# Performance work log

Hardware: AMD Instinct MI355X
Metric: run time of the kernel (lower is better)

## Reference

```python
import jax, jax.numpy as jnp
import numpy as np

ROI = 7      # pooled output size
S = 5        # max adaptive samples per bin dim (boxes <= 0.25*120=30px -> ceil(30/7)=5)


def _roi_align(f, boxes):
    """torchvision roi_align, aligned=True, sampling_ratio=-1 (adaptive).
    f: [C,H,W]; boxes: [N,4] normalized xywh. Returns [N,C,ROI,ROI]."""
    C, H, W = f.shape
    fH, fW = jnp.float32(H), jnp.float32(W)
    x1 = boxes[:, 0] * fW - 0.5                 # aligned=True offset
    y1 = boxes[:, 1] * fH - 0.5
    roi_w = boxes[:, 2] * fW
    roi_h = boxes[:, 3] * fH
    bin_w = roi_w / ROI
    bin_h = roi_h / ROI
    gw = jnp.maximum(jnp.ceil(roi_w / ROI), 1.0)   # adaptive grid counts [N]
    gh = jnp.maximum(jnp.ceil(roi_h / ROI), 1.0)
    ph = jnp.arange(ROI, dtype=jnp.float32)
    s = jnp.arange(S, dtype=jnp.float32)
    # sample coords [N, ROI, S]
    ys = y1[:, None, None] + ph[None, :, None] * bin_h[:, None, None] \
         + (s[None, None, :] + 0.5) * bin_h[:, None, None] / gh[:, None, None]
    xs = x1[:, None, None] + ph[None, :, None] * bin_w[:, None, None] \
         + (s[None, None, :] + 0.5) * bin_w[:, None, None] / gw[:, None, None]
    # broadcast to [N, ROI, ROI, S, S]
    y = ys[:, :, None, :, None]
    x = xs[:, None, :, None, :]
    m = ((s[None, None, None, :, None] < gh[:, None, None, None, None]) &
         (s[None, None, None, None, :] < gw[:, None, None, None, None]))
    valid = (y > -1.0) & (y < fH) & (x > -1.0) & (x < fW)
    yc = jnp.clip(y, 0.0, fH - 1.0)
    xc = jnp.clip(x, 0.0, fW - 1.0)
    y0 = jnp.floor(yc).astype(jnp.int32)
    x0 = jnp.floor(xc).astype(jnp.int32)
    yh = jnp.minimum(y0 + 1, H - 1)
    xh = jnp.minimum(x0 + 1, W - 1)
    ly = yc - y0.astype(jnp.float32); hy = 1.0 - ly
    lx = xc - x0.astype(jnp.float32); hx = 1.0 - lx
    scale = (valid & m).astype(f.dtype)
    y = jnp.broadcast_to(y0 * 0, (boxes.shape[0], ROI, ROI, S, S))  # shape anchor (unused)
    w00 = (hy * hx * scale)[None]
    w01 = (hy * lx * scale)[None]
    w10 = (ly * hx * scale)[None]
    w11 = (ly * lx * scale)[None]
    # gathered values: [C, N, ROI, ROI, S, S]
    vals = (w00 * f[:, y0, x0] + w01 * f[:, y0, xh] +
            w10 * f[:, yh, x0] + w11 * f[:, yh, xh])
    count = (gh * gw)[None, :, None, None]
    pooled = vals.sum(axis=(-1, -2)) / count        # [C, N, ROI, ROI]
    return pooled.transpose(1, 0, 2, 3)              # [N, C, ROI, ROI]


def setup_inputs() -> dict:
    key = jax.random.key(0)
    k = jax.random.split(key, 6)
    features = jax.random.normal(k[0], (1, 128, 120, 120), jnp.float32)
    u = jax.random.uniform(k[1], (512, 4), jnp.float32)
    boxes = jnp.stack([u[:, 0] * 0.7, u[:, 1] * 0.7,
                       0.05 + 0.2 * u[:, 2], 0.05 + 0.2 * u[:, 3]], axis=1)
    d_in = 128 * ROI * ROI  # 6272
    W1 = jax.random.normal(k[2], (d_in, 512), jnp.float32) / np.float32(np.sqrt(d_in))
    b1 = jax.random.normal(k[3], (512,), jnp.float32) * 0.01
    W2 = jax.random.normal(k[4], (512, 256), jnp.float32) / np.float32(np.sqrt(512))
    b2 = jax.random.normal(k[5], (256,), jnp.float32) * 0.01
    return {"features": features, "boxes": boxes, "W1": W1, "b1": b1, "W2": W2, "b2": b2}


def reference(features, boxes, W1, b1, W2, b2):
    roi = _roi_align(features[0], boxes)             # [N,128,7,7]
    flat = roi.reshape(roi.shape[0], -1)             # [N,6272] channel-major like torch .view
    h = jax.nn.relu(flat @ W1 + b1)                  # dropout in eval mode = identity
    return h @ W2 + b2                               # [N,256]
```

## Files before the change

### kernel.cpp

```cpp
#include <hip/hip_runtime.h>
#include <hip/hip_bf16.h>
#include <stdint.h>

#define DI __device__ __forceinline__

typedef __attribute__((ext_vector_type(8))) short short8;
typedef __attribute__((ext_vector_type(4))) float f32x4;

constexpr int CH   = 128;
constexpr int FH   = 120;
constexpr int FW   = 120;
constexpr int NBOX = 512;
constexpr int KDIM = 49 * 128;
constexpr int D1   = 512;
constexpr int D2   = 256;
constexpr int SPLITS = 14;
constexpr int KC     = KDIM / SPLITS;

DI float bf2f(uint32_t u16) { union { uint32_t i; float f; } v; v.i = u16 << 16; return v.f; }
DI float bf2f_hi(uint32_t u) { union { uint32_t i; float f; } v; v.i = u & 0xffff0000u; return v.f; }
DI uint16_t f2bf(float f) {
    __hip_bfloat16 h = __float2bfloat16(f);
    union { __hip_bfloat16 h; uint16_t u; } v; v.h = h; return v.u;
}

__global__ __launch_bounds__(256) void k_preft(const float* __restrict__ f,
                                               uint32_t* __restrict__ ft) {
    __shared__ float lds[30 * 129];
    const int v = blockIdx.x, t = threadIdx.x;
    const int y = v >> 2, x0 = (v & 3) * 30;
    for (int e = t; e < 30 * 128; e += 256) {
        int c = e / 30, x = e - c * 30;
        lds[x * 129 + c] = f[c * (FH * FW) + y * FW + x0 + x];
    }
    __syncthreads();
    for (int e = t; e < 30 * 64; e += 256) {
        int x = e >> 6, cp = e & 63;
        float lo = lds[x * 129 + 2 * cp];
        float hi = lds[x * 129 + 2 * cp + 1];
        ft[(y * FW + x0 + x) * 64 + cp] = (uint32_t)f2bf(lo) | ((uint32_t)f2bf(hi) << 16);
    }
}

template<int GH, int GW>
DI void roi_body(const uint32_t* __restrict__ ft, uint32_t* __restrict__ A,
                 int wid, int lane,
                 const float (*__restrict__ tyv)[4], const float (*__restrict__ txv)[4],
                 int ph, int pw, float cnt) {
#pragma clang fp contract(off)
    const int q = lane >> 4, cg = lane & 15;
    const int qx = q & 1, qy = q >> 1;
    int offx[GW];
    float wx[GW];
#pragma unroll
    for (int j = 0; j < GW; ++j) {
        const float* e = txv[pw * 5 + j];
        wx[j]   = qx ? e[1] : e[0];
        offx[j] = __float_as_int(qx ? e[3] : e[2]) + 4 * cg;
    }
    int offy[GH];
    float wy[GH];
#pragma unroll
    for (int s = 0; s < GH; ++s) {
        const float* e = tyv[ph * 5 + s];
        wy[s]   = qy ? e[1] : e[0];
        offy[s] = __float_as_int(qy ? e[3] : e[2]);
    }

    float acc[8] = {};
    if constexpr (GH * GW <= 12) {
        uint4 u[GH][GW];
#pragma unroll
        for (int s = 0; s < GH; ++s)
#pragma unroll
            for (int j = 0; j < GW; ++j)
                u[s][j] = *(const uint4*)(ft + offy[s] + offx[j]);
#pragma unroll
        for (int s = 0; s < GH; ++s)
#pragma unroll
            for (int j = 0; j < GW; ++j) {
                const float w = wy[s] * wx[j];
                acc[0] += w * bf2f(u[s][j].x & 0xffffu); acc[1] += w * bf2f_hi(u[s][j].x);
                acc[2] += w * bf2f(u[s][j].y & 0xffffu); acc[3] += w * bf2f_hi(u[s][j].y);
                acc[4] += w * bf2f(u[s][j].z & 0xffffu); acc[5] += w * bf2f_hi(u[s][j].z);
                acc[6] += w * bf2f(u[s][j].w & 0xffffu); acc[7] += w * bf2f_hi(u[s][j].w);
            }
    } else {
#pragma unroll
        for (int s = 0; s < GH; ++s) {
            uint4 u[GW];
#pragma unroll
            for (int j = 0; j < GW; ++j)
                u[j] = *(const uint4*)(ft + offy[s] + offx[j]);
#pragma unroll
            for (int j = 0; j < GW; ++j) {
                const float w = wy[s] * wx[j];
                acc[0] += w * bf2f(u[j].x & 0xffffu); acc[1] += w * bf2f_hi(u[j].x);
                acc[2] += w * bf2f(u[j].y & 0xffffu); acc[3] += w * bf2f_hi(u[j].y);
                acc[4] += w * bf2f(u[j].z & 0xffffu); acc[5] += w * bf2f_hi(u[j].z);
                acc[6] += w * bf2f(u[j].w & 0xffffu); acc[7] += w * bf2f_hi(u[j].w);
            }
        }
    }
    float tot[8];
#pragma unroll
    for (int i = 0; i < 8; ++i) {
        float v16 = acc[i] + __shfl_xor(acc[i], 16);
        tot[i] = v16 + __shfl_xor(v16, 32);
    }
    if (q == 0) {
        uint4 pk;
        pk.x = (uint32_t)f2bf(tot[0] / cnt) | ((uint32_t)f2bf(tot[1] / cnt) << 16);
        pk.y = (uint32_t)f2bf(tot[2] / cnt) | ((uint32_t)f2bf(tot[3] / cnt) << 16);
        pk.z = (uint32_t)f2bf(tot[4] / cnt) | ((uint32_t)f2bf(tot[5] / cnt) << 16);
        pk.w = (uint32_t)f2bf(tot[6] / cnt) | ((uint32_t)f2bf(tot[7] / cnt) << 16);
        *(uint4*)(A + (size_t)wid * 64 + 4 * cg) = pk;
    }
}

__global__ __launch_bounds__(256) void k_roi_w(const uint32_t* __restrict__ ft,
                                               const float* __restrict__ boxes,
                                               const float* __restrict__ W1,
                                               const float* __restrict__ W2,
                                               uint32_t* __restrict__ A,
                                               uint16_t* __restrict__ W1rT,
                                               uint16_t* __restrict__ W2T) {
    __shared__ __align__(16) float lds[128 * 33];
    __shared__ __align__(16) float tyv[35][4];
    __shared__ __align__(16) float txv[35][4];
    const int blk = blockIdx.x, t = threadIdx.x;
    if (blk < 6656) {
#pragma clang fp contract(off)
        const int box = blk / 13, quad = blk % 13;
        const float bx = boxes[box * 4 + 0], by = boxes[box * 4 + 1];
        const float bw = boxes[box * 4 + 2], bh = boxes[box * 4 + 3];
        const float x1 = bx * 120.0f - 0.5f;
        const float y1 = by * 120.0f - 0.5f;
        const float roi_w = bw * 120.0f, roi_h = bh * 120.0f;
        const float bin_w = roi_w / 7.0f, bin_h = roi_h / 7.0f;
        const float gwf = fmaxf(ceilf(roi_w / 7.0f), 1.0f);
        const float ghf = fmaxf(ceilf(roi_h / 7.0f), 1.0f);
        const int gwi = (int)gwf, ghi = (int)ghf;
        const float cnt = ghf * gwf;

        if (t < 35) {
            const int ph = t / 5, sy = t % 5;
            float yy = (y1 + (float)ph * bin_h) + ((float)sy + 0.5f) * bin_h / ghf;
            float my = ((yy > -1.0f) && (yy < 120.0f)) ? 1.0f : 0.0f;
            float yc = fminf(fmaxf(yy, 0.0f), 119.0f);
            int y0 = (int)floorf(yc);
            int yh = min(y0 + 1, 119);
            float ly = yc - (float)y0, hy = 1.0f - ly;
            tyv[t][0] = hy * my;
            tyv[t][1] = ly * my;
            tyv[t][2] = __int_as_float(y0 * (FW * 64));
            tyv[t][3] = __int_as_float(yh * (FW * 64));
        } else if (t < 70) {
            const int u = t - 35;
            const int pw = u / 5, sx = u % 5;
            float xx = (x1 + (float)pw * bin_w) + ((float)sx + 0.5f) * bin_w / gwf;
            float mx = ((xx > -1.0f) && (xx < 120.0f)) ? 1.0f : 0.0f;
            float xc = fminf(fmaxf(xx, 0.0f), 119.0f);
            int x0 = (int)floorf(xc);
            int xh = min(x0 + 1, 119);
            float lx = xc - (float)x0, hx = 1.0f - lx;
            txv[u][0] = hx * mx;
            txv[u][1] = lx * mx;
            txv[u][2] = __int_as_float(x0 * 64);
            txv[u][3] = __int_as_float(xh * 64);
        }
        __syncthreads();

        const int w8 = t >> 6, lane = t & 63;
        const int bin = quad * 4 + w8;
        if (bin < 49) {
            const int ph = bin / 7, pw = bin - ph * 7;
            const int wid = box * 49 + bin;
#define RB(GH, GW) roi_body<GH, GW>(ft, A, wid, lane, tyv, txv, ph, pw, cnt)
            switch (ghi * 8 + gwi) {
            case  9: RB(1,1); break; case 10: RB(1,2); break; case 11: RB(1,3); break;
            case 12: RB(1,4); break; case 13: RB(1,5); break;
            case 17: RB(2,1); break; case 18: RB(2,2); break; case 19: RB(2,3); break;
            case 20: RB(2,4); break; case 21: RB(2,5); break;
            case 25: RB(3,1); break; case 26: RB(3,2); break; case 27: RB(3,3); break;
            case 28: RB(3,4); break; case 29: RB(3,5); break;
            case 33: RB(4,1); break; case 34: RB(4,2); break; case 35: RB(4,3); break;
            case 36: RB(4,4); break; case 37: RB(4,5); break;
            case 41: RB(5,1); break; case 42: RB(5,2); break; case 43: RB(5,3); break;
            case 44: RB(5,4); break; default: RB(5,5); break;
            }
#undef RB
        }
    } else if (blk < 7440) {
        const int vb = blk - 6656;
        const int b = vb % 49, j0 = (vb / 49) * 32;
        for (int e = t; e < 4096; e += 256) {
            int ci = e >> 5, jj = e & 31;
            lds[ci * 33 + jj] = W1[(ci * 49 + b) * D1 + j0 + jj];
        }
        __syncthreads();
        for (int e = t; e < 4096; e += 256) {
            int jj = e >> 7, ci = e & 127;
            W1rT[(size_t)(j0 + jj) * KDIM + b * 128 + ci] = f2bf(lds[ci * 33 + jj]);
        }
    } else {
        const int v2 = blk - 7440;
        const int n0 = (v2 & 7) * 32, k0 = (v2 >> 3) * 128;
        for (int e = t; e < 4096; e += 256) {
            int k = e >> 5, nn = e & 31;
            lds[k * 33 + nn] = W2[(k0 + k) * D2 + n0 + nn];
        }
        __syncthreads();
        for (int e = t; e < 4096; e += 256) {
            int nn = e >> 7, k = e & 127;
            W2T[(n0 + nn) * D1 + k0 + k] = f2bf(lds[k * 33 + nn]);
        }
    }
}

__global__ __launch_bounds__(256) void k_gemm1(const uint16_t* __restrict__ A,
                                               const uint16_t* __restrict__ B,
                                               float* __restrict__ P) {
    __shared__ __align__(16) uint16_t As[64 * 32];
    __shared__ __align__(16) uint16_t Bs[64 * 32];
    const int id = blockIdx.x;
    const int nid = (id & 7) * 112 + (id >> 3);
    const int bz = nid >> 6;
    const int r64 = nid & 63;
    const int m0 = (r64 >> 3) * 64, n0 = (r64 & 7) * 64;
    const int kbase = bz * KC;
    const int t = threadIdx.x;
    const int lane = t & 63, w = t >> 6;
    const int wr = w >> 1, wc = w & 1;

    f32x4 acc[2][2] = {};
    const int kb = lane >> 4, r16 = lane & 15;
    const int row = t >> 2, c8 = t & 3;
    const int ldst = row * 32 + ((c8 ^ ((row >> 1) & 3)) * 8);
    const uint16_t* ga = A + (size_t)(m0 + row) * KDIM + c8 * 8;
    const uint16_t* gb = B + (size_t)(n0 + row) * KDIM + c8 * 8;

    for (int ks = 0; ks < KC / 32; ++ks) {
        const int kk = kbase + ks * 32;
        __syncthreads();
        *(uint4*)&As[ldst] = *(const uint4*)&ga[kk];
        *(uint4*)&Bs[ldst] = *(const uint4*)&gb[kk];
        __syncthreads();

        short8 af[2], bfr[2];
#pragma unroll
        for (int mi = 0; mi < 2; ++mi) {
            int ar = wr * 32 + mi * 16 + r16;
            af[mi] = *(const short8*)&As[ar * 32 + (kb ^ ((ar >> 1) & 3)) * 8];
        }
#pragma unroll
        for (int ni = 0; ni < 2; ++ni) {
            int br = wc * 32 + ni * 16 + r16;
            bfr[ni] = *(const short8*)&Bs[br * 32 + (kb ^ ((br >> 1) & 3)) * 8];
        }
#pragma unroll
        for (int mi = 0; mi < 2; ++mi)
#pragma unroll
            for (int ni = 0; ni < 2; ++ni)
                acc[mi][ni] = __builtin_amdgcn_mfma_f32_16x16x32_bf16(af[mi], bfr[ni], acc[mi][ni], 0, 0, 0);
    }

    float* outp = P + (size_t)bz * (D1 * D1);
#pragma unroll
    for (int mi = 0; mi < 2; ++mi)
#pragma unroll
        for (int ni = 0; ni < 2; ++ni) {
            int rrow = m0 + wr * 32 + mi * 16 + kb * 4;
            int ccol = n0 + wc * 32 + ni * 16 + r16;
#pragma unroll
            for (int r = 0; r < 4; ++r)
                outp[(size_t)(rrow + r) * D1 + ccol] = acc[mi][ni][r];
        }
}

__global__ __launch_bounds__(256) void k_reduce1(const float* __restrict__ P,
                                                 const float* __restrict__ b1,
                                                 uint16_t* __restrict__ Hm) {
    const int e4 = blockIdx.x * 256 + threadIdx.x;
    const f32x4* P4 = (const f32x4*)P;
    f32x4 s = {};
#pragma unroll
    for (int i = 0; i < SPLITS; ++i) s += P4[(size_t)i * (D1 * D1 / 4) + e4];
    const int c4 = (e4 & 127) * 4;
    uint16_t h[4];
#pragma unroll
    for (int j = 0; j < 4; ++j) h[j] = f2bf(fmaxf(s[j] + b1[c4 + j], 0.0f));
    uint2 pk;
    pk.x = (uint32_t)h[0] | ((uint32_t)h[1] << 16);
    pk.y = (uint32_t)h[2] | ((uint32_t)h[3] << 16);
    *(uint2*)&Hm[(size_t)e4 * 4] = pk;
}

__global__ __launch_bounds__(256) void k_gemm2(const uint16_t* __restrict__ Hm,
                                               const uint16_t* __restrict__ W2T,
                                               const float* __restrict__ b2,
                                               float* __restrict__ out) {
    const int wid  = blockIdx.x * 4 + (threadIdx.x >> 6);
    const int lane = threadIdx.x & 63;
    const int mt = wid >> 4, nt = wid & 15;
    const int m0 = mt * 16, n0 = nt * 16;
    const int g = lane >> 4, i = lane & 15;
    f32x4 acc = {};
#pragma unroll
    for (int kk = 0; kk < D1 / 32; ++kk) {
        short8 a = *(const short8*)&Hm[(m0 + i) * D1 + kk * 32 + g * 8];
        short8 b = *(const short8*)&W2T[(n0 + i) * D1 + kk * 32 + g * 8];
        acc = __builtin_amdgcn_mfma_f32_16x16x32_bf16(a, b, acc, 0, 0, 0);
    }
    const float bias = b2[n0 + i];
#pragma unroll
    for (int r = 0; r < 4; ++r)
        out[(size_t)(m0 + g * 4 + r) * D2 + n0 + i] = acc[r] + bias;
}

extern "C" void kernel_launch(void* const* d_in, const int* in_sizes, int n_in,
                              void* d_out, int out_size, void* d_ws, size_t ws_size,
                              hipStream_t stream) {
    const float* f     = (const float*)d_in[0];
    const float* boxes = (const float*)d_in[1];
    const float* W1    = (const float*)d_in[2];
    const float* b1    = (const float*)d_in[3];
    const float* W2    = (const float*)d_in[4];
    const float* b2    = (const float*)d_in[5];
    float* out = (float*)d_out;

    char* p = (char*)d_ws;
    uint32_t* ft   = (uint32_t*)p; p += (size_t)FH * FW * (CH / 2) * 4;
    uint16_t* W1rT = (uint16_t*)p; p += (size_t)D1 * KDIM * 2;
    uint16_t* W2T  = (uint16_t*)p; p += (size_t)D2 * D1 * 2;
    uint16_t* Ar   = (uint16_t*)p; p += (size_t)NBOX * KDIM * 2;
    float*    Pp   = (float*)p;    p += (size_t)SPLITS * D1 * D1 * 4;
    uint16_t* Hm   = (uint16_t*)p; p += (size_t)D1 * D1 * 2;

    k_preft<<<480, 256, 0, stream>>>(f, ft);
    k_roi_w<<<7472, 256, 0, stream>>>(ft, boxes, W1, W2, (uint32_t*)Ar, W1rT, W2T);
    k_gemm1<<<896, 256, 0, stream>>>(Ar, W1rT, Pp);
    k_reduce1<<<D1 * D1 / 4 / 256, 256, 0, stream>>>(Pp, b1, Hm);
    k_gemm2<<<(D1 / 16) * (D2 / 16) / 4, 256, 0, stream>>>(Hm, W2T, b2, out);
}
```

Measured before the change: 60.68 us.

## Enlarge GEMM1 tiles to 128x128 and load tiles directly into LDS

The split-K GEMM1 kernel now computes 128x128 output tiles per block (4x4 MFMA fragments per wave) instead of 64x64, and launches 224 blocks instead of 896. Global-to-LDS staging uses the global_load_lds builtin, with the XOR swizzle moved to the global source address. The aim is more operand reuse per LDS load and no trip through registers for tile loads. In exchange, 224 blocks may underfill the GPU's CUs, and register pressure rises.

Result: slower. 63.13 us (+4.0%).

```diff
diff --git a/kernel.cpp b/kernel.cpp
--- a/kernel.cpp
+++ b/kernel.cpp
@@ -22,6 +22,12 @@
 DI uint16_t f2bf(float f) {
     __hip_bfloat16 h = __float2bfloat16(f);
     union { __hip_bfloat16 h; uint16_t u; } v; v.h = h; return v.u;
+}
+
+typedef __attribute__((address_space(3))) uint32_t lds_u32;
+typedef const __attribute__((address_space(1))) uint32_t glb_u32;
+DI void gload16(const void* g, void* l) {
+    __builtin_amdgcn_global_load_lds((glb_u32*)g, (lds_u32*)l, 16, 0, 0);
 }
 
 __global__ __launch_bounds__(256) void k_preft(const float* __restrict__ f,
@@ -221,57 +227,68 @@
 __global__ __launch_bounds__(256) void k_gemm1(const uint16_t* __restrict__ A,
                                                const uint16_t* __restrict__ B,
                                                float* __restrict__ P) {
-    __shared__ __align__(16) uint16_t As[64 * 32];
-    __shared__ __align__(16) uint16_t Bs[64 * 32];
+    __shared__ __align__(16) uint16_t As[128 * 32];
+    __shared__ __align__(16) uint16_t Bs[128 * 32];
     const int id = blockIdx.x;
-    const int nid = (id & 7) * 112 + (id >> 3);
-    const int bz = nid >> 6;
-    const int r64 = nid & 63;
-    const int m0 = (r64 >> 3) * 64, n0 = (r64 & 7) * 64;
+    const int nid = (id & 7) * 28 + (id >> 3);
+    const int bz = nid >> 4;
+    const int r16t = nid & 15;
+    const int m0 = (r16t >> 2) * 128, n0 = (r16t & 3) * 128;
     const int kbase = bz * KC;
     const int t = threadIdx.x;
     const int lane = t & 63, w = t >> 6;
     const int wr = w >> 1, wc = w & 1;
 
-    f32x4 acc[2][2] = {};
+    f32x4 acc[4][4] = {};
     const int kb = lane >> 4, r16 = lane & 15;
-    const int row = t >> 2, c8 = t & 3;
-    const int ldst = row * 32 + ((c8 ^ ((row >> 1) & 3)) * 8);
-    const uint16_t* ga = A + (size_t)(m0 + row) * KDIM + c8 * 8;
-    const uint16_t* gb = B + (size_t)(n0 + row) * KDIM + c8 * 8;
+
+    const int row0 = t >> 2, c8p0 = t & 3;
+    const int sw0 = (row0 >> 1) & 3;
+    const uint16_t* gA0 = A + (size_t)(m0 + row0) * KDIM + (c8p0 ^ sw0) * 8;
+    const uint16_t* gB0 = B + (size_t)(n0 + row0) * KDIM + (c8p0 ^ sw0) * 8;
+    const int row1 = (t + 256) >> 2, c8p1 = t & 3;
+    const int sw1 = (row1 >> 1) & 3;
+    const uint16_t* gA1 = A + (size_t)(m0 + row1) * KDIM + (c8p1 ^ sw1) * 8;
+    const uint16_t* gB1 = B + (size_t)(n0 + row1) * KDIM + (c8p1 ^ sw1) * 8;
+    uint16_t* dA0 = As + (size_t)t * 8;
+    uint16_t* dA1 = As + (size_t)(t + 256) * 8;
+    uint16_t* dB0 = Bs + (size_t)t * 8;
+    uint16_t* dB1 = Bs + (size_t)(t + 256) * 8;
 
     for (int ks = 0; ks < KC / 32; ++ks) {
         const int kk = kbase + ks * 32;
         __syncthreads();
-        *(uint4*)&As[ldst] = *(const uint4*)&ga[kk];
-        *(uint4*)&Bs[ldst] = *(const uint4*)&gb[kk];
-        __syncthreads();
-
-        short8 af[2], bfr[2];
-#pragma unroll
-        for (int mi = 0; mi < 2; ++mi) {
-            int ar = wr * 32 + mi * 16 + r16;
+        gload16(gA0 + kk, dA0);
+        gload16(gA1 + kk, dA1);
+        gload16(gB0 + kk, dB0);
+        gload16(gB1 + kk, dB1);
+        __syncthreads();
+
+        short8 af[4], bfr[4];
+#pragma unroll
+        for (int mi = 0; mi < 4; ++mi) {
+            int ar = wr * 64 + mi * 16 + r16;
             af[mi] = *(const short8*)&As[ar * 32 + (kb ^ ((ar >> 1) & 3)) * 8];
         }
 #pragma unroll
-        for (int ni = 0; ni < 2; ++ni) {
-            int br = wc * 32 + ni * 16 + r16;
+        for (int ni = 0; ni < 4; ++ni) {
+            int br = wc * 64 + ni * 16 + r16;
             bfr[ni] = *(const short8*)&Bs[br * 32 + (kb ^ ((br >> 1) & 3)) * 8];
         }
 #pragma unroll
-        for (int mi = 0; mi < 2; ++mi)
-#pragma unroll
-            for (int ni = 0; ni < 2; ++ni)
+        for (int mi = 0; mi < 4; ++mi)
+#pragma unroll
+            for (int ni = 0; ni < 4; ++ni)
                 acc[mi][ni] = __builtin_amdgcn_mfma_f32_16x16x32_bf16(af[mi], bfr[ni], acc[mi][ni], 0, 0, 0);
     }
 
     float* outp = P + (size_t)bz * (D1 * D1);
 #pragma unroll
-    for (int mi = 0; mi < 2; ++mi)
-#pragma unroll
-        for (int ni = 0; ni < 2; ++ni) {
-            int rrow = m0 + wr * 32 + mi * 16 + kb * 4;
-            int ccol = n0 + wc * 32 + ni * 16 + r16;
+    for (int mi = 0; mi < 4; ++mi)
+#pragma unroll
+        for (int ni = 0; ni < 4; ++ni) {
+            int rrow = m0 + wr * 64 + mi * 16 + kb * 4;
+            int ccol = n0 + wc * 64 + ni * 16 + r16;
 #pragma unroll
             for (int r = 0; r < 4; ++r)
                 outp[(size_t)(rrow + r) * D1 + ccol] = acc[mi][ni][r];
@@ -339,7 +356,7 @@
 
     k_preft<<<480, 256, 0, stream>>>(f, ft);
     k_roi_w<<<7472, 256, 0, stream>>>(ft, boxes, W1, W2, (uint32_t*)Ar, W1rT, W2T);
-    k_gemm1<<<896, 256, 0, stream>>>(Ar, W1rT, Pp);
+    k_gemm1<<<224, 256, 0, stream>>>(Ar, W1rT, Pp);
     k_reduce1<<<D1 * D1 / 4 / 256, 256, 0, stream>>>(Pp, b1, Hm);
     k_gemm2<<<(D1 / 16) * (D2 / 16) / 4, 256, 0, stream>>>(Hm, W2T, b2, out);
 }
```
